# Kernel optimization log

Measured on AMD Instinct MI355X. Metric: run time of the kernel, lower is better.

Reference implementation:

```python
import jax, jax.numpy as jnp
import numpy as np

N_DIM, D_SKETCH, M_COLS = 8192, 1024, 4096


def setup_inputs() -> dict:
    key = jax.random.key(0)
    kM, kD, kP = jax.random.split(key, 3)
    M = jax.random.normal(kM, (N_DIM, M_COLS), dtype=jnp.float32)
    # Rademacher signs, exactly as 2*(rand > 0.5).float() - 1
    D = 2.0 * (jax.random.uniform(kD, (N_DIM,)) > 0.5).astype(jnp.float32) - 1.0
    # np.random.choice(N, d) samples with replacement -> plain randint
    P = jax.random.randint(kP, (D_SKETCH,), 0, N_DIM)
    return {"M": M, "D": D, "P": P}


def _idct_rows(X, rows):
    # torch_dct.idct with norm=None along the last axis, evaluated only at the
    # output positions `rows` (identical values to full idct followed by gather):
    #   x[n] = (1/N) * ( X[...,0]/2 + sum_{k=1}^{N-1} X[...,k] * cos(pi*(2n+1)*k/(2N)) )
    N = X.shape[-1]
    k = jnp.arange(N, dtype=jnp.float32)
    w = jnp.where(k == 0, 0.5, 1.0) / N                      # DCT-III weights / N
    n = rows.astype(jnp.float32)
    ang = (jnp.pi / (2.0 * N)) * (2.0 * n[:, None] + 1.0) * k[None, :]
    C = jnp.cos(ang) * w[None, :]                            # [d, N]
    return jnp.einsum('dk,mk->md', C, X)                     # [m, d]


def reference(M, D, P):
    # SRFT sketch, 2-D branch, transpose=False:
    #   result = idct((D[:, None] * M).T).T[P, :]   ->  shape [d, m]
    X = D[:, None] * M                                       # sign flip, [N, m]
    out = _idct_rows(X.T, P)                                 # [m, d]
    return out.T                                             # [d, m]
```

## Files before the change

### kernel.cpp

```cpp
#include <hip/hip_runtime.h>

#define K_DIM 8192
#define M_OUT 1024
#define N_OUT 4096
#define BUFSZ 65536

typedef __attribute__((ext_vector_type(4))) float f32x4;
typedef __attribute__((ext_vector_type(8))) __bf16 bf16x8;
typedef __attribute__((ext_vector_type(2))) __bf16 bf16x2;
typedef __attribute__((ext_vector_type(4))) unsigned u32x4;
typedef __attribute__((ext_vector_type(8))) unsigned short u16x8;

__device__ __forceinline__ unsigned short f2bf(float x) {
  unsigned u = __builtin_bit_cast(unsigned, x);
  u += 0x7fffu + ((u >> 16) & 1u);
  return (unsigned short)(u >> 16);
}

__device__ __forceinline__ unsigned pack2(float a, float b) {
  bf16x2 v;
  v[0] = (__bf16)a;
  v[1] = (__bf16)b;
  return __builtin_bit_cast(unsigned, v);
}

__global__ __launch_bounds__(256) void build_c_kernel(
    const int* __restrict__ Pp, const float* __restrict__ Dp,
    unsigned short* __restrict__ Cm) {
  const int p = blockIdx.x;
  const int n2 = 2 * Pp[p] + 1;
  const int t = threadIdx.x;
#pragma unroll
  for (int ch = 0; ch < 4; ++ch) {
    const int kb = (ch << 11) + (t << 3);
    u16x8 o;
#pragma unroll
    for (int i = 0; i < 8; ++i) {
      const int k = kb + i;
      const unsigned tt = ((unsigned)(n2 * k)) & 32767u;
      const float cv = cosf((float)tt * 1.9174759848570515e-4f);
      const float wk = (k == 0) ? (0.5f / 8192.0f) : (1.0f / 8192.0f);
      o[i] = f2bf(cv * wk * Dp[k]);
    }
    *(u16x8*)(Cm + ((size_t)p << 13) + kb) = o;
  }
}

__global__ __launch_bounds__(512, 1) void gemm_kernel(
    const unsigned short* __restrict__ Cm, const float* __restrict__ Mp,
    float* __restrict__ outp, int kchunk, int nwg) {
  __shared__ __align__(16) char lds[2 * BUFSZ];

  const int id = blockIdx.x;
  const int chunk = nwg >> 3;
  const int sid = (id & 7) * chunk + (id >> 3);
  const int bm = sid & 3, bn = (sid >> 2) & 15, bz = sid >> 6;

  const int t = threadIdx.x;
  const int w = t >> 6, l = t & 63;
  const int wr = w >> 2, wc = w & 3;
  const int lg = l >> 4, lr = l & 15;
  const int k_begin = bz * kchunk;
  const int NT = kchunk >> 6;

  const int arow = t >> 3;
  const int acol = ((t & 7) << 4) ^ ((arow & 7) << 4);
  const char* Agl = (const char*)Cm + ((size_t)(bm * 256 + arow) << 14) +
                    ((size_t)k_begin << 1) + acol;
  auto stageA = [&](int nbuf, int tile) {
    char* d = (char*)lds + nbuf * BUFSZ + t * 16;
    const char* s = Agl + ((size_t)tile << 7);
#pragma unroll
    for (int i = 0; i < 4; ++i)
      __builtin_amdgcn_global_load_lds(
          (const __attribute__((address_space(1))) void*)(s + ((size_t)i << 20)),
          (__attribute__((address_space(3))) void*)(d + i * 8192), 16, 0, 0);
  };

  const float* Bg = Mp + (size_t)k_begin * N_OUT + bn * 256 + l * 4;
  auto loadB = [&](f32x4 (&r)[8], int tile, int half) {
#pragma unroll
    for (int i = 0; i < 4; ++i)
      r[half * 4 + i] =
          *(const f32x4*)(Bg + (size_t)(tile * 64 + w * 8 + half * 4 + i) * N_OUT);
  };
  auto writeB = [&](const f32x4 (&r)[8], int nbuf, int nn) {
    const int n = (l << 2) + nn;
    const int sN = (n & 7) ^ ((n >> 2) & 7);
    u32x4 pk;
#pragma unroll
    for (int j = 0; j < 4; ++j) pk[j] = pack2(r[2 * j][nn], r[2 * j + 1][nn]);
    *(u32x4*)(lds + nbuf * BUFSZ + 32768 + n * 128 + ((w ^ sN) << 4)) = pk;
  };

  const int sw = (lr & 7) << 4;
  const int xk0 = (lg << 4) ^ sw;
  const int xk1 = (64 + (lg << 4)) ^ sw;
  unsigned boff[2][4];
#pragma unroll
  for (int kk = 0; kk < 2; ++kk)
#pragma unroll
    for (int nf = 0; nf < 4; ++nf) {
      const int row = wc * 64 + nf * 16 + lr;
      const int sN = (row & 7) ^ ((row >> 2) & 7);
      boff[kk][nf] = 32768 + row * 128 + ((((kk << 2) | lg) ^ sN) << 4);
    }

  f32x4 acc[8][4] = {};
  bf16x8 Af[4];
  bf16x8 Bf[4];

  auto readA = [&](const char* aBuf, int mh, int xk) {
#pragma unroll
    for (int m = 0; m < 4; ++m)
      Af[m] = *(const bf16x8*)(aBuf + mh * 8192 + m * 2048 + xk);
  };
  auto readB = [&](int nbuf, int kk) {
#pragma unroll
    for (int nf = 0; nf < 4; ++nf)
      Bf[nf] = *(const bf16x8*)(lds + nbuf * BUFSZ + boff[kk][nf]);
  };
  auto mm = [&](int mh) {
    __builtin_amdgcn_s_setprio(1);
#pragma unroll
    for (int m = 0; m < 4; ++m)
#pragma unroll
      for (int nf = 0; nf < 4; ++nf)
        acc[mh * 4 + m][nf] = __builtin_amdgcn_mfma_f32_16x16x32_bf16(
            Af[m], Bf[nf], acc[mh * 4 + m][nf], 0, 0, 0);
    __builtin_amdgcn_s_setprio(0);
  };

  {
    f32x4 p[8];
    stageA(0, 0);
    loadB(p, 0, 0);
    loadB(p, 0, 1);
#pragma unroll
    for (int nn = 0; nn < 4; ++nn) writeB(p, 0, nn);
    asm volatile("s_waitcnt vmcnt(0) lgkmcnt(0)" ::: "memory");
    __builtin_amdgcn_sched_barrier(0);
    __builtin_amdgcn_s_barrier();
  }

  for (int tt = 0; tt < NT; ++tt) {
    const int cur = tt & 1, nxt = cur ^ 1;
    const char* aBuf = (const char*)lds + cur * BUFSZ + wr * 16384 + lr * 128;
    const bool more = (tt + 1) < NT;
    f32x4 sb[8];
    if (more) {
      loadB(sb, tt + 1, 0);
      loadB(sb, tt + 1, 1);
    }
    readB(cur, 0);
    readA(aBuf, 0, xk0);
    __builtin_amdgcn_s_barrier();
    mm(0);
    __builtin_amdgcn_s_barrier();
    readA(aBuf, 1, xk0);
    if (more) stageA(nxt, tt + 1);
    __builtin_amdgcn_s_barrier();
    mm(1);
    __builtin_amdgcn_s_barrier();
    readB(cur, 1);
    readA(aBuf, 0, xk1);
    __builtin_amdgcn_s_barrier();
    mm(0);
    __builtin_amdgcn_s_barrier();
    readA(aBuf, 1, xk1);
    if (more) {
      writeB(sb, nxt, 0);
      writeB(sb, nxt, 1);
      writeB(sb, nxt, 2);
      writeB(sb, nxt, 3);
    }
    __builtin_amdgcn_s_barrier();
    mm(1);
    asm volatile("s_waitcnt vmcnt(0) lgkmcnt(0)" ::: "memory");
    __builtin_amdgcn_sched_barrier(0);
    __builtin_amdgcn_s_barrier();
  }

  float* po = outp + (size_t)bz * (M_OUT * N_OUT);
  const int orow = bm * 256 + wr * 128;
  const int ocol = bn * 256 + wc * 64 + lr;
#pragma unroll
  for (int mi = 0; mi < 8; ++mi) {
    const int r0 = orow + (mi >> 2) * 64 + (mi & 3) * 16 + (lg << 2);
#pragma unroll
    for (int ni = 0; ni < 4; ++ni) {
      const int c = ocol + ni * 16;
#pragma unroll
      for (int q = 0; q < 4; ++q)
        po[(size_t)(r0 + q) * N_OUT + c] = acc[mi][ni][q];
    }
  }
}

__global__ __launch_bounds__(256) void reduce_kernel(
    const float* __restrict__ part, float* __restrict__ out, int ksplit) {
  const size_t total = (size_t)M_OUT * N_OUT;
  const size_t i = ((size_t)blockIdx.x * 256 + threadIdx.x) * 4;
  if (i >= total) return;
  f32x4 s = *(const f32x4*)(part + i);
  for (int s2 = 1; s2 < ksplit; ++s2) s += *(const f32x4*)(part + (size_t)s2 * total + i);
  *(f32x4*)(out + i) = s;
}

__global__ __launch_bounds__(256) void naive_kernel(
    const float* __restrict__ Mp, const float* __restrict__ Dp,
    const int* __restrict__ Pp, float* __restrict__ out) {
  const int p = blockIdx.y;
  const int j = blockIdx.x * 256 + threadIdx.x;
  const int n2 = 2 * Pp[p] + 1;
  float acc = 0.0f;
  for (int k = 0; k < K_DIM; ++k) {
    const unsigned tt = ((unsigned)(n2 * k)) & 32767u;
    const float cv = cosf((float)tt * 1.9174759848570515e-4f);
    const float wk = (k == 0) ? 0.5f : 1.0f;
    acc += cv * wk * Dp[k] * Mp[(size_t)k * N_OUT + j];
  }
  out[(size_t)p * N_OUT + j] = acc * (1.0f / 8192.0f);
}

extern "C" void kernel_launch(void* const* d_in, const int* in_sizes, int n_in,
                              void* d_out, int out_size, void* d_ws, size_t ws_size,
                              hipStream_t stream) {
  const float* Mp = (const float*)d_in[0];
  const float* Dp = (const float*)d_in[1];
  const int* Pp = (const int*)d_in[2];
  float* out = (float*)d_out;

  const size_t CM_BYTES = (size_t)M_OUT * K_DIM * 2;
  const size_t PART_BYTES = (size_t)M_OUT * N_OUT * 4;

  int ksplit;
  if (ws_size >= CM_BYTES + 4 * PART_BYTES) ksplit = 4;
  else if (ws_size >= CM_BYTES + 2 * PART_BYTES) ksplit = 2;
  else if (ws_size >= CM_BYTES) ksplit = 1;
  else ksplit = 0;

  if (ksplit == 0) {
    naive_kernel<<<dim3(N_OUT / 256, M_OUT), 256, 0, stream>>>(Mp, Dp, Pp, out);
    return;
  }

  unsigned short* Cm = (unsigned short*)d_ws;
  float* part = (float*)((char*)d_ws + CM_BYTES);

  build_c_kernel<<<dim3(M_OUT), 256, 0, stream>>>(Pp, Dp, Cm);

  float* gout = (ksplit > 1) ? part : out;
  const int kchunk = K_DIM / ksplit;
  const int nwg = 64 * ksplit;
  gemm_kernel<<<dim3(nwg), 512, 0, stream>>>(Cm, Mp, gout, kchunk, nwg);

  if (ksplit > 1)
    reduce_kernel<<<dim3((M_OUT * N_OUT / 4 + 255) / 256), 256, 0, stream>>>(part, out, ksplit);
}
```

Baseline: 112.6 us.

## Prefetch B tiles two iterations ahead with ping-pong register buffers

Restructures the GEMM main loop so global loads of the fp32 M tile are issued two K-tiles ahead into alternating register buffers, with partial vmcnt waits. The A-tile LDS stage moves to the start of each iteration and the B write to LDS moves earlier. The aim is to hide global memory latency for B behind more MFMA work. In exchange it uses more registers (a second 8×f32x4 buffer), which could cause spills, and the vmcnt(8) accounting interleaved with the global_load_lds calls is delicate.

```diff
diff --git a/kernel.cpp b/kernel.cpp
--- a/kernel.cpp
+++ b/kernel.cpp
@@ -78,19 +78,21 @@
   };
 
   const float* Bg = Mp + (size_t)k_begin * N_OUT + bn * 256 + l * 4;
-  auto loadB = [&](f32x4 (&r)[8], int tile, int half) {
-#pragma unroll
-    for (int i = 0; i < 4; ++i)
-      r[half * 4 + i] =
-          *(const f32x4*)(Bg + (size_t)(tile * 64 + w * 8 + half * 4 + i) * N_OUT);
-  };
-  auto writeB = [&](const f32x4 (&r)[8], int nbuf, int nn) {
-    const int n = (l << 2) + nn;
-    const int sN = (n & 7) ^ ((n >> 2) & 7);
-    u32x4 pk;
-#pragma unroll
-    for (int j = 0; j < 4; ++j) pk[j] = pack2(r[2 * j][nn], r[2 * j + 1][nn]);
-    *(u32x4*)(lds + nbuf * BUFSZ + 32768 + n * 128 + ((w ^ sN) << 4)) = pk;
+  auto loadB = [&](f32x4 (&r)[8], int tile) {
+#pragma unroll
+    for (int i = 0; i < 8; ++i)
+      r[i] = *(const f32x4*)(Bg + (size_t)(tile * 64 + w * 8 + i) * N_OUT);
+  };
+  auto writeB = [&](const f32x4 (&r)[8], int nbuf) {
+#pragma unroll
+    for (int nn = 0; nn < 4; ++nn) {
+      const int n = (l << 2) + nn;
+      const int sN = (n & 7) ^ ((n >> 2) & 7);
+      u32x4 pk;
+#pragma unroll
+      for (int j = 0; j < 4; ++j) pk[j] = pack2(r[2 * j][nn], r[2 * j + 1][nn]);
+      *(u32x4*)(lds + nbuf * BUFSZ + 32768 + n * 128 + ((w ^ sN) << 4)) = pk;
+    }
   };
 
   const int sw = (lr & 7) << 4;
@@ -131,54 +133,53 @@
     __builtin_amdgcn_s_setprio(0);
   };
 
+  f32x4 sbA[8], sbB[8];
+
   {
-    f32x4 p[8];
     stageA(0, 0);
-    loadB(p, 0, 0);
-    loadB(p, 0, 1);
-#pragma unroll
-    for (int nn = 0; nn < 4; ++nn) writeB(p, 0, nn);
-    asm volatile("s_waitcnt vmcnt(0) lgkmcnt(0)" ::: "memory");
+    loadB(sbA, 0);
+    loadB(sbB, 1);
+    writeB(sbA, 0);
+    asm volatile("s_waitcnt vmcnt(8) lgkmcnt(0)" ::: "memory");
     __builtin_amdgcn_sched_barrier(0);
     __builtin_amdgcn_s_barrier();
   }
 
-  for (int tt = 0; tt < NT; ++tt) {
+  auto tile_body = [&](int tt, f32x4 (&sbLoad)[8], f32x4 (&sbWrite)[8]) {
     const int cur = tt & 1, nxt = cur ^ 1;
     const char* aBuf = (const char*)lds + cur * BUFSZ + wr * 16384 + lr * 128;
-    const bool more = (tt + 1) < NT;
-    f32x4 sb[8];
-    if (more) {
-      loadB(sb, tt + 1, 0);
-      loadB(sb, tt + 1, 1);
-    }
+    const bool more1 = (tt + 1) < NT;
+    const bool more2 = (tt + 2) < NT;
+    if (more1) stageA(nxt, tt + 1);
     readB(cur, 0);
     readA(aBuf, 0, xk0);
     __builtin_amdgcn_s_barrier();
     mm(0);
     __builtin_amdgcn_s_barrier();
+    if (more2) loadB(sbLoad, tt + 2);
     readA(aBuf, 1, xk0);
-    if (more) stageA(nxt, tt + 1);
     __builtin_amdgcn_s_barrier();
     mm(1);
     __builtin_amdgcn_s_barrier();
     readB(cur, 1);
     readA(aBuf, 0, xk1);
+    if (more1) writeB(sbWrite, nxt);
     __builtin_amdgcn_s_barrier();
     mm(0);
     __builtin_amdgcn_s_barrier();
     readA(aBuf, 1, xk1);
-    if (more) {
-      writeB(sb, nxt, 0);
-      writeB(sb, nxt, 1);
-      writeB(sb, nxt, 2);
-      writeB(sb, nxt, 3);
-    }
     __builtin_amdgcn_s_barrier();
     mm(1);
-    asm volatile("s_waitcnt vmcnt(0) lgkmcnt(0)" ::: "memory");
+    if (more2) { asm volatile("s_waitcnt vmcnt(8)" ::: "memory"); }
+    else       { asm volatile("s_waitcnt vmcnt(0)" ::: "memory"); }
+    asm volatile("s_waitcnt lgkmcnt(0)" ::: "memory");
     __builtin_amdgcn_sched_barrier(0);
     __builtin_amdgcn_s_barrier();
+  };
+
+  for (int tt = 0; tt < NT; tt += 2) {
+    tile_body(tt, sbA, sbB);
+    tile_body(tt + 1, sbB, sbA);
   }
 
   float* po = outp + (size_t)bz * (M_OUT * N_OUT);
```

Measured after the change: 316.4 us. 2.81x slower.
